# Performance work log

Measured on AMD Instinct MI355X. Metric: run time of the kernel, lower is better.

Reference implementation:

```python
import jax, jax.numpy as jnp
import numpy as np

TAU = 0.25
VTH = 1.0

def setup_inputs() -> dict:
    key = jax.random.key(0)
    k1, k2 = jax.random.split(key)
    B, T, F, U = 256, 100, 1024, 1024
    x = jax.random.normal(k1, (B, T, F), dtype=jnp.float32)
    kernel = jax.random.normal(k2, (F, U), dtype=jnp.float32) * 0.02
    bias = jnp.zeros((U,), dtype=jnp.float32)
    return {"x": x, "kernel": kernel, "bias": bias}

def reference(x, kernel, bias):
    # x: [B, T, F]; one big GEMM for all timesteps, then sequential LIF scan.
    current = jnp.einsum('btf,fu->btu', x, kernel) + bias  # [B, T, U]
    B, T, U = current.shape
    v0 = jnp.zeros((B, U), dtype=x.dtype)

    def lif_step(voltage, cur_t):
        voltage = TAU * voltage + (1.0 - TAU) * cur_t
        spikes = (voltage > VTH).astype(cur_t.dtype)
        voltage = voltage - spikes * VTH
        return voltage, spikes

    _, spikes_t = jax.lax.scan(lif_step, v0, jnp.moveaxis(current, 1, 0))  # [T, B, U]
    output_spikes = jnp.moveaxis(spikes_t, 0, 1)  # [B, T, U]
    spike_counts = jnp.sum(output_spikes, axis=1)  # [B, U]
    return output_spikes, spike_counts
```

## Files before the change

### kernel.cpp

```cpp
#include <hip/hip_runtime.h>


#define UN 128
#define BK 16
#define CS 132
#define CHUNK 50
#define TMAX 100

__device__ __forceinline__ void gload_lds16(const float* g, float* l) {
    __builtin_amdgcn_global_load_lds(
        (const __attribute__((address_space(1))) void*)g,
        (__attribute__((address_space(3))) void*)l,
        16, 0, 0);
}

__global__ __launch_bounds__(256) void fused_snn(
    const float* __restrict__ x,
    const float* __restrict__ W,
    const float* __restrict__ bias,
    float* __restrict__ spikes,
    float* __restrict__ counts,
    int B, int T, int F, int U)
{
    __shared__ __align__(16) float smem[CHUNK * CS];
    float* As0 = smem;
    float* As1 = smem + 1600;

    const int tid = threadIdx.x;
    const int tg  = tid >> 4;
    const int ug  = tid & 15;
    const int u0  = blockIdx.x * UN;
    const int b   = blockIdx.y;

    float acc[7][8];
    #pragma unroll
    for (int i = 0; i < 7; i++)
        #pragma unroll
        for (int j = 0; j < 8; j++) acc[i][j] = 0.f;

    const float* xb = x + (size_t)b * T * F;

    const float* ga0 = xb + (size_t)(tid >> 2) * F + (tid & 3) * 4;
    const float* ga1 = xb + (size_t)(64 + (tid >> 2)) * F + (tid & 3) * 4;
    const int la0 = tid * 4;
    const int la1 = (256 + tid) * 4;
    const bool a1on = (tid < 144);
    const bool w0   = (tid < 64);

#define STAGE(buf, kof)                                   \
    do {                                                  \
        gload_lds16(ga0 + (kof), (buf) + la0);            \
        if (a1on) gload_lds16(ga1 + (kof), (buf) + la1);  \
    } while (0)

#define COMPUTE(buf, k0b)                                                  \
    do {                                                                   \
        const float* ap = (buf) + tg * 16;                                 \
        _Pragma("unroll 1")                                                \
        for (int kk = 0; kk < BK; kk += 2) {                               \
            const float* wk = W + (size_t)((k0b) + kk) * U + u0;           \
            float4 b0 = *(const float4*)(wk + 4 * ug);                     \
            float4 b1 = *(const float4*)(wk + 64 + 4 * ug);                \
            float4 b2 = *(const float4*)(wk + U + 4 * ug);                 \
            float4 b3 = *(const float4*)(wk + U + 64 + 4 * ug);            \
            _Pragma("unroll")                                              \
            for (int i = 0; i < 6; i++) {                                  \
                float2 a = *(const float2*)(ap + i * 256 + kk);            \
                acc[i][0] += a.x * b0.x;  acc[i][1] += a.x * b0.y;         \
                acc[i][2] += a.x * b0.z;  acc[i][3] += a.x * b0.w;         \
                acc[i][4] += a.x * b1.x;  acc[i][5] += a.x * b1.y;         \
                acc[i][6] += a.x * b1.z;  acc[i][7] += a.x * b1.w;         \
                acc[i][0] += a.y * b2.x;  acc[i][1] += a.y * b2.y;         \
                acc[i][2] += a.y * b2.z;  acc[i][3] += a.y * b2.w;         \
                acc[i][4] += a.y * b3.x;  acc[i][5] += a.y * b3.y;         \
                acc[i][6] += a.y * b3.z;  acc[i][7] += a.y * b3.w;         \
            }                                                              \
            if (w0) {     \
                float2 a = *(const float2*)(ap + 6 * 256 + kk);            \
                acc[6][0] += a.x * b0.x;  acc[6][1] += a.x * b0.y;         \
                acc[6][2] += a.x * b0.z;  acc[6][3] += a.x * b0.w;         \
                acc[6][4] += a.x * b1.x;  acc[6][5] += a.x * b1.y;         \
                acc[6][6] += a.x * b1.z;  acc[6][7] += a.x * b1.w;         \
                acc[6][0] += a.y * b2.x;  acc[6][1] += a.y * b2.y;         \
                acc[6][2] += a.y * b2.z;  acc[6][3] += a.y * b2.w;         \
                acc[6][4] += a.y * b3.x;  acc[6][5] += a.y * b3.y;         \
                acc[6][6] += a.y * b3.z;  acc[6][7] += a.y * b3.w;         \
            }                                                              \
        }                                                                  \
    } while (0)

    STAGE(As0, 0);
    __syncthreads();

    #pragma unroll 1
    for (int k0 = 0; k0 < F; k0 += 2 * BK) {
        STAGE(As1, k0 + BK);
        COMPUTE(As0, k0);
        __syncthreads();
        if (k0 + 2 * BK < F) STAGE(As0, k0 + 2 * BK);
        COMPUTE(As1, k0 + BK);
        __syncthreads();
    }

#undef STAGE
#undef COMPUTE

    float bb[8];
    {
        float4 bv0 = *(const float4*)(bias + u0 + 4 * ug);
        float4 bv1 = *(const float4*)(bias + u0 + 64 + 4 * ug);
        bb[0] = bv0.x; bb[1] = bv0.y; bb[2] = bv0.z; bb[3] = bv0.w;
        bb[4] = bv1.x; bb[5] = bv1.y; bb[6] = bv1.z; bb[7] = bv1.w;
    }

    float v = 0.f, cnt = 0.f;
    float* sp = spikes + (size_t)b * T * U + u0 + tid;

    #pragma unroll
    for (int c = 0; c < 2; c++) {
        #pragma unroll
        for (int i = 0; i < 7; i++) {
            const int t = i * 16 + tg;
            if (t >= c * CHUNK && t < c * CHUNK + CHUNK && t < TMAX) {
                const int r = t - c * CHUNK;
                float4 c0, c1;
                c0.x = acc[i][0] + bb[0]; c0.y = acc[i][1] + bb[1];
                c0.z = acc[i][2] + bb[2]; c0.w = acc[i][3] + bb[3];
                c1.x = acc[i][4] + bb[4]; c1.y = acc[i][5] + bb[5];
                c1.z = acc[i][6] + bb[6]; c1.w = acc[i][7] + bb[7];
                *(float4*)(smem + r * CS + 4 * ug)      = c0;
                *(float4*)(smem + r * CS + 64 + 4 * ug) = c1;
            }
        }
        __syncthreads();
        if (tid < UN) {
#pragma clang fp contract(off)
            for (int r = 0; r < CHUNK; r++) {
                float cval = smem[r * CS + tid];
                v = 0.25f * v + 0.75f * cval;
                float s = (v > 1.0f) ? 1.0f : 0.0f;
                v -= s;
                cnt += s;
                sp[(size_t)(c * CHUNK + r) * U] = s;
            }
        }
        __syncthreads();
    }
    if (tid < UN) counts[(size_t)b * U + u0 + tid] = cnt;
}

extern "C" void kernel_launch(void* const* d_in, const int* in_sizes, int n_in,
                              void* d_out, int out_size, void* d_ws, size_t ws_size,
                              hipStream_t stream) {
    const float* x    = (const float*)d_in[0];
    const float* kern = (const float*)d_in[1];
    const float* bias = (const float*)d_in[2];
    float* out = (float*)d_out;

    const int U = in_sizes[2];
    const int F = in_sizes[1] / U;
    const int R = in_sizes[0] / F;
    const int B = out_size / U - R;
    const int T = R / B;

    float* spikes = out;
    float* counts = out + (size_t)R * U;

    dim3 grid(U / UN, B);
    fused_snn<<<grid, 256, 0, stream>>>(x, kern, bias, spikes, counts,
                                        B, T, F, U);
}
```

Before: 850.6 us.

## Widen block tile to 256 units and stage weights in LDS

Each block now covers 256 output units, with each thread holding a 7x16 accumulator tile. Weight rows are copied into double-buffered LDS with async global-to-LDS loads instead of being read per thread from global memory. The LIF scan now uses all 256 threads over four 25-step chunks. This is meant to raise arithmetic intensity and cut redundant global weight traffic, at the cost of more registers per thread (lower occupancy) and half as many blocks.

```diff
diff --git a/kernel.cpp b/kernel.cpp
--- a/kernel.cpp
+++ b/kernel.cpp
@@ -1,10 +1,10 @@
 #include <hip/hip_runtime.h>
 
 
-#define UN 128
+#define UN 256
 #define BK 16
-#define CS 132
-#define CHUNK 50
+#define CSS 264
+#define CHUNK 25
 #define TMAX 100
 
 __device__ __forceinline__ void gload_lds16(const float* g, float* l) {
@@ -22,9 +22,11 @@
     float* __restrict__ counts,
     int B, int T, int F, int U)
 {
-    __shared__ __align__(16) float smem[CHUNK * CS];
+    __shared__ __align__(16) float smem[11392];
     float* As0 = smem;
     float* As1 = smem + 1600;
+    float* Ws0 = smem + 3200;
+    float* Ws1 = smem + 7296;
 
     const int tid = threadIdx.x;
     const int tg  = tid >> 4;
@@ -32,11 +34,11 @@
     const int u0  = blockIdx.x * UN;
     const int b   = blockIdx.y;
 
-    float acc[7][8];
+    float acc[7][16];
     #pragma unroll
     for (int i = 0; i < 7; i++)
         #pragma unroll
-        for (int j = 0; j < 8; j++) acc[i][j] = 0.f;
+        for (int j = 0; j < 16; j++) acc[i][j] = 0.f;
 
     const float* xb = x + (size_t)b * T * F;
 
@@ -47,106 +49,146 @@
     const bool a1on = (tid < 144);
     const bool w0   = (tid < 64);
 
-#define STAGE(buf, kof)                                   \
-    do {                                                  \
-        gload_lds16(ga0 + (kof), (buf) + la0);            \
-        if (a1on) gload_lds16(ga1 + (kof), (buf) + la1);  \
+    const float* gwr = W + (size_t)(tid >> 6) * U + u0 + (tid & 63) * 4;
+    const int lw = tid * 4;
+
+#define STAGE(abuf, wbuf, kof)                                          \
+    do {                                                                \
+        gload_lds16(ga0 + (kof), (abuf) + la0);                         \
+        if (a1on) gload_lds16(ga1 + (kof), (abuf) + la1);               \
+        _Pragma("unroll")                                               \
+        for (int r = 0; r < 4; r++)                                     \
+            gload_lds16(gwr + (size_t)((kof) + 4 * r) * U,              \
+                        (wbuf) + lw + r * 1024);                        \
     } while (0)
 
-#define COMPUTE(buf, k0b)                                                  \
-    do {                                                                   \
-        const float* ap = (buf) + tg * 16;                                 \
-        _Pragma("unroll 1")                                                \
-        for (int kk = 0; kk < BK; kk += 2) {                               \
-            const float* wk = W + (size_t)((k0b) + kk) * U + u0;           \
-            float4 b0 = *(const float4*)(wk + 4 * ug);                     \
-            float4 b1 = *(const float4*)(wk + 64 + 4 * ug);                \
-            float4 b2 = *(const float4*)(wk + U + 4 * ug);                 \
-            float4 b3 = *(const float4*)(wk + U + 64 + 4 * ug);            \
-            _Pragma("unroll")                                              \
-            for (int i = 0; i < 6; i++) {                                  \
-                float2 a = *(const float2*)(ap + i * 256 + kk);            \
-                acc[i][0] += a.x * b0.x;  acc[i][1] += a.x * b0.y;         \
-                acc[i][2] += a.x * b0.z;  acc[i][3] += a.x * b0.w;         \
-                acc[i][4] += a.x * b1.x;  acc[i][5] += a.x * b1.y;         \
-                acc[i][6] += a.x * b1.z;  acc[i][7] += a.x * b1.w;         \
-                acc[i][0] += a.y * b2.x;  acc[i][1] += a.y * b2.y;         \
-                acc[i][2] += a.y * b2.z;  acc[i][3] += a.y * b2.w;         \
-                acc[i][4] += a.y * b3.x;  acc[i][5] += a.y * b3.y;         \
-                acc[i][6] += a.y * b3.z;  acc[i][7] += a.y * b3.w;         \
-            }                                                              \
-            if (w0) {     \
-                float2 a = *(const float2*)(ap + 6 * 256 + kk);            \
-                acc[6][0] += a.x * b0.x;  acc[6][1] += a.x * b0.y;         \
-                acc[6][2] += a.x * b0.z;  acc[6][3] += a.x * b0.w;         \
-                acc[6][4] += a.x * b1.x;  acc[6][5] += a.x * b1.y;         \
-                acc[6][6] += a.x * b1.z;  acc[6][7] += a.x * b1.w;         \
-                acc[6][0] += a.y * b2.x;  acc[6][1] += a.y * b2.y;         \
-                acc[6][2] += a.y * b2.z;  acc[6][3] += a.y * b2.w;         \
-                acc[6][4] += a.y * b3.x;  acc[6][5] += a.y * b3.y;         \
-                acc[6][6] += a.y * b3.z;  acc[6][7] += a.y * b3.w;         \
-            }                                                              \
-        }                                                                  \
+#define FMA16(i, av, r0, r1, r2, r3)                                    \
+    do {                                                                \
+        acc[i][0]  += (av) * r0.x;  acc[i][1]  += (av) * r0.y;          \
+        acc[i][2]  += (av) * r0.z;  acc[i][3]  += (av) * r0.w;          \
+        acc[i][4]  += (av) * r1.x;  acc[i][5]  += (av) * r1.y;          \
+        acc[i][6]  += (av) * r1.z;  acc[i][7]  += (av) * r1.w;          \
+        acc[i][8]  += (av) * r2.x;  acc[i][9]  += (av) * r2.y;          \
+        acc[i][10] += (av) * r2.z;  acc[i][11] += (av) * r2.w;          \
+        acc[i][12] += (av) * r3.x;  acc[i][13] += (av) * r3.y;          \
+        acc[i][14] += (av) * r3.z;  acc[i][15] += (av) * r3.w;          \
     } while (0)
 
-    STAGE(As0, 0);
+#define COMPUTE(abuf, wbuf)                                             \
+    do {                                                                \
+        const float* ap  = (abuf) + tg * 16;                            \
+        const float* wpk = (wbuf) + ug * 8;                             \
+        _Pragma("unroll 1")                                             \
+        for (int kk = 0; kk < BK; kk += 2) {                            \
+            float2 a0 = *(const float2*)(ap + 0 * 256 + kk);            \
+            float2 a1 = *(const float2*)(ap + 1 * 256 + kk);            \
+            float2 a2 = *(const float2*)(ap + 2 * 256 + kk);            \
+            float2 a3 = *(const float2*)(ap + 3 * 256 + kk);            \
+            float2 a4 = *(const float2*)(ap + 4 * 256 + kk);            \
+            float2 a5 = *(const float2*)(ap + 5 * 256 + kk);            \
+            float2 a6;                                                  \
+            if (w0) a6 = *(const float2*)(ap + 6 * 256 + kk);           \
+            {                                               \
+                const float* wr = wpk + kk * 256;                       \
+                float4 p0 = *(const float4*)(wr);                       \
+                float4 p1 = *(const float4*)(wr + 4);                   \
+                float4 p2 = *(const float4*)(wr + 128);                 \
+                float4 p3 = *(const float4*)(wr + 132);                 \
+                FMA16(0, a0.x, p0, p1, p2, p3);                         \
+                FMA16(1, a1.x, p0, p1, p2, p3);                         \
+                FMA16(2, a2.x, p0, p1, p2, p3);                         \
+                FMA16(3, a3.x, p0, p1, p2, p3);                         \
+                FMA16(4, a4.x, p0, p1, p2, p3);                         \
+                FMA16(5, a5.x, p0, p1, p2, p3);                         \
+                if (w0) { FMA16(6, a6.x, p0, p1, p2, p3); }             \
+            }                                                           \
+            {                                             \
+                const float* wr = wpk + (kk + 1) * 256;                 \
+                float4 q0 = *(const float4*)(wr);                       \
+                float4 q1 = *(const float4*)(wr + 4);                   \
+                float4 q2 = *(const float4*)(wr + 128);                 \
+                float4 q3 = *(const float4*)(wr + 132);                 \
+                FMA16(0, a0.y, q0, q1, q2, q3);                         \
+                FMA16(1, a1.y, q0, q1, q2, q3);                         \
+                FMA16(2, a2.y, q0, q1, q2, q3);                         \
+                FMA16(3, a3.y, q0, q1, q2, q3);                         \
+                FMA16(4, a4.y, q0, q1, q2, q3);                         \
+                FMA16(5, a5.y, q0, q1, q2, q3);                         \
+                if (w0) { FMA16(6, a6.y, q0, q1, q2, q3); }             \
+            }                                                           \
+        }                                                               \
+    } while (0)
+
+    STAGE(As0, Ws0, 0);
     __syncthreads();
 
     #pragma unroll 1
     for (int k0 = 0; k0 < F; k0 += 2 * BK) {
-        STAGE(As1, k0 + BK);
-        COMPUTE(As0, k0);
-        __syncthreads();
-        if (k0 + 2 * BK < F) STAGE(As0, k0 + 2 * BK);
-        COMPUTE(As1, k0 + BK);
+        STAGE(As1, Ws1, k0 + BK);
+        COMPUTE(As0, Ws0);
+        __syncthreads();
+        if (k0 + 2 * BK < F) STAGE(As0, Ws0, k0 + 2 * BK);
+        COMPUTE(As1, Ws1);
         __syncthreads();
     }
 
 #undef STAGE
 #undef COMPUTE
-
-    float bb[8];
+#undef FMA16
+
+    float bb[16];
     {
-        float4 bv0 = *(const float4*)(bias + u0 + 4 * ug);
-        float4 bv1 = *(const float4*)(bias + u0 + 64 + 4 * ug);
-        bb[0] = bv0.x; bb[1] = bv0.y; bb[2] = bv0.z; bb[3] = bv0.w;
-        bb[4] = bv1.x; bb[5] = bv1.y; bb[6] = bv1.z; bb[7] = bv1.w;
+        float4 b0 = *(const float4*)(bias + u0 + ug * 8);
+        float4 b1 = *(const float4*)(bias + u0 + ug * 8 + 4);
+        float4 b2 = *(const float4*)(bias + u0 + 128 + ug * 8);
+        float4 b3 = *(const float4*)(bias + u0 + 128 + ug * 8 + 4);
+        bb[0]=b0.x; bb[1]=b0.y; bb[2]=b0.z; bb[3]=b0.w;
+        bb[4]=b1.x; bb[5]=b1.y; bb[6]=b1.z; bb[7]=b1.w;
+        bb[8]=b2.x; bb[9]=b2.y; bb[10]=b2.z; bb[11]=b2.w;
+        bb[12]=b3.x; bb[13]=b3.y; bb[14]=b3.z; bb[15]=b3.w;
     }
 
-    float v = 0.f, cnt = 0.f;
+    float vv = 0.f, cnt = 0.f;
     float* sp = spikes + (size_t)b * T * U + u0 + tid;
 
     #pragma unroll
-    for (int c = 0; c < 2; c++) {
+    for (int c = 0; c < 4; c++) {
         #pragma unroll
         for (int i = 0; i < 7; i++) {
             const int t = i * 16 + tg;
             if (t >= c * CHUNK && t < c * CHUNK + CHUNK && t < TMAX) {
                 const int r = t - c * CHUNK;
-                float4 c0, c1;
-                c0.x = acc[i][0] + bb[0]; c0.y = acc[i][1] + bb[1];
-                c0.z = acc[i][2] + bb[2]; c0.w = acc[i][3] + bb[3];
-                c1.x = acc[i][4] + bb[4]; c1.y = acc[i][5] + bb[5];
-                c1.z = acc[i][6] + bb[6]; c1.w = acc[i][7] + bb[7];
-                *(float4*)(smem + r * CS + 4 * ug)      = c0;
-                *(float4*)(smem + r * CS + 64 + 4 * ug) = c1;
+                float4 d0, d1, d2, d3;
+                d0.x = acc[i][0]  + bb[0];  d0.y = acc[i][1]  + bb[1];
+                d0.z = acc[i][2]  + bb[2];  d0.w = acc[i][3]  + bb[3];
+                d1.x = acc[i][4]  + bb[4];  d1.y = acc[i][5]  + bb[5];
+                d1.z = acc[i][6]  + bb[6];  d1.w = acc[i][7]  + bb[7];
+                d2.x = acc[i][8]  + bb[8];  d2.y = acc[i][9]  + bb[9];
+                d2.z = acc[i][10] + bb[10]; d2.w = acc[i][11] + bb[11];
+                d3.x = acc[i][12] + bb[12]; d3.y = acc[i][13] + bb[13];
+                d3.z = acc[i][14] + bb[14]; d3.w = acc[i][15] + bb[15];
+                float* row = smem + r * CSS;
+                *(float4*)(row + ug * 8)           = d0;
+                *(float4*)(row + ug * 8 + 4)       = d1;
+                *(float4*)(row + 128 + ug * 8)     = d2;
+                *(float4*)(row + 128 + ug * 8 + 4) = d3;
             }
         }
         __syncthreads();
-        if (tid < UN) {
+        {
 #pragma clang fp contract(off)
             for (int r = 0; r < CHUNK; r++) {
-                float cval = smem[r * CS + tid];
-                v = 0.25f * v + 0.75f * cval;
-                float s = (v > 1.0f) ? 1.0f : 0.0f;
-                v -= s;
+                float cval = smem[r * CSS + tid];
+                vv = 0.25f * vv + 0.75f * cval;
+                float s = (vv > 1.0f) ? 1.0f : 0.0f;
+                vv -= s;
                 cnt += s;
                 sp[(size_t)(c * CHUNK + r) * U] = s;
             }
         }
         __syncthreads();
     }
-    if (tid < UN) counts[(size_t)b * U + u0 + tid] = cnt;
+    counts[(size_t)b * U + u0 + tid] = cnt;
 }
 
 extern "C" void kernel_launch(void* const* d_in, const int* in_sizes, int n_in,
```

Measured after the change: 764.6 us. 1.11x faster.
